# Optimization experiments

Hardware: AMD Instinct MI355X
Metric: run time of the kernel (lower is better)

The kernel has to match this reference:

```python
import jax, jax.numpy as jnp
import numpy as np

# dims: M=512 new tokens, N=2048 model dim, D=128 head dim, H=16 heads,
# L=4096 cache length, P=2048 cache write offset

def setup_inputs() -> dict:
    key = jax.random.key(0)
    k0, k1, k2, k3 = jax.random.split(key, 4)
    M, N, D, L = 512, 2048, 128, 4096
    X = jax.random.normal(k0, (M, N), jnp.float32)
    # scale weights ~1/sqrt(N) so projections have unit-ish scale
    W_qkv = jax.random.normal(k1, (N, 3 * N), jnp.float32) * (N ** -0.5)
    H = N // D
    cache_K = jax.random.normal(k2, (H, L, D), jnp.float32)
    # realistic cache state: keys stored in cache are RMS-normalized
    cache_K = cache_K * jax.lax.rsqrt(jnp.mean(cache_K * cache_K, axis=-1, keepdims=True))
    cache_V = jax.random.normal(k3, (H, L, D), jnp.float32)
    return {"X": X, "W_qkv": W_qkv, "cache_K": cache_K, "cache_V": cache_V, "P": 2048}


def reference(X, W_qkv, cache_K, cache_V, P):
    M = X.shape[0]
    H, L, D = cache_K.shape
    qkv = X @ W_qkv                              # [M, 3N]
    q, k, v = jnp.split(qkv, 3, axis=-1)         # each [M, N]
    q = q.reshape(M, H, D).transpose(1, 0, 2)    # [H, M, D]
    k = k.reshape(M, H, D).transpose(1, 0, 2)
    v = v.reshape(M, H, D).transpose(1, 0, 2)
    # RMS-style normalization (no learned gain, no eps in original)
    q = q * jax.lax.rsqrt(jnp.mean(q * q, axis=-1, keepdims=True))
    k = k * jax.lax.rsqrt(jnp.mean(k * k, axis=-1, keepdims=True))
    # scatter-update into KV cache at position P
    Kc = jax.lax.dynamic_update_slice(cache_K, k, (0, P, 0))  # [H, L, D]
    Vc = jax.lax.dynamic_update_slice(cache_V, v, (0, P, 0))
    # unmasked, unscaled attention over the full cache (faithful to original:
    # plain exp/sum, no max-subtraction, no 1/sqrt(D))
    scores = jnp.einsum('hmd,hld->hml', q, Kc)   # [H, M, L]
    w = jnp.exp(scores)
    w = w / jnp.sum(w, axis=-1, keepdims=True)
    out = jnp.einsum('hml,hld->hmd', w, Vc)      # [H, M, D]
    return out.transpose(1, 0, 2).reshape(M, H * D)
```

## Files before the change

### kernel.cpp

```cpp
#include <hip/hip_runtime.h>
#include <math.h>

typedef _Float16 half_t;
typedef _Float16 half8 __attribute__((ext_vector_type(8)));
typedef _Float16 half4_t __attribute__((ext_vector_type(4)));
typedef _Float16 half2_t __attribute__((ext_vector_type(2)));
typedef float floatx4 __attribute__((ext_vector_type(4)));

#define M_TOK 512
#define N_DIM 2048
#define D_HEAD 128
#define H_HEADS 16
#define L_CACHE 4096
#define THREE_N 6144
#define NCHUNK 16
#define LCHUNK 256

__global__ __launch_bounds__(256) void prep_kernel(const float* __restrict__ cK,
                                                   const float* __restrict__ cV,
                                                   const float* __restrict__ W,
                                                   const float* __restrict__ X,
                                                   half_t* __restrict__ K16,
                                                   half_t* __restrict__ V16T,
                                                   half_t* __restrict__ W16T,
                                                   half_t* __restrict__ X16) {
    __shared__ half_t tile[32 * 36];
    int b = blockIdx.x;
    int t = threadIdx.x;

    if (b < 8192) {
        size_t i = ((size_t)b * 256 + t) * 4;
        float4 v = *(const float4*)(cK + i);
        half4_t h = {(half_t)v.x, (half_t)v.y, (half_t)v.z, (half_t)v.w};
        *(half4_t*)(K16 + i) = h;
        return;
    }
    b -= 8192;
    if (b < 1024) {
        size_t i = ((size_t)b * 256 + t) * 4;
        float4 v = *(const float4*)(X + i);
        half4_t h = {(half_t)v.x, (half_t)v.y, (half_t)v.z, (half_t)v.w};
        *(half4_t*)(X16 + i) = h;
        return;
    }
    b -= 1024;
    if (b < 8192) {
        int h = b >> 9;
        int rem = b & 511;
        int lt = rem >> 2, dt = rem & 3;
        int l0 = lt * 32, d0 = dt * 32;
        {
            int li = t >> 3, c4 = (t & 7) * 4;
            float4 v = *(const float4*)(cV + ((size_t)h * L_CACHE + l0 + li) * D_HEAD + d0 + c4);
            tile[li * 36 + c4 + 0] = (half_t)v.x;
            tile[li * 36 + c4 + 1] = (half_t)v.y;
            tile[li * 36 + c4 + 2] = (half_t)v.z;
            tile[li * 36 + c4 + 3] = (half_t)v.w;
        }
        __syncthreads();
        {
            int di = t >> 3, lj = (t & 7) * 4;
            half4_t o = {tile[(lj + 0) * 36 + di], tile[(lj + 1) * 36 + di],
                         tile[(lj + 2) * 36 + di], tile[(lj + 3) * 36 + di]};
            *(half4_t*)(V16T + ((size_t)h * D_HEAD + d0 + di) * L_CACHE + l0 + lj) = o;
        }
        return;
    }
    b -= 8192;
    {
        int n0 = (b % 192) * 32, k0 = (b / 192) * 32;
        {
            int ki = t >> 3, n4 = (t & 7) * 4;
            float4 v = *(const float4*)(W + (size_t)(k0 + ki) * THREE_N + n0 + n4);
            tile[ki * 36 + n4 + 0] = (half_t)v.x;
            tile[ki * 36 + n4 + 1] = (half_t)v.y;
            tile[ki * 36 + n4 + 2] = (half_t)v.z;
            tile[ki * 36 + n4 + 3] = (half_t)v.w;
        }
        __syncthreads();
        {
            int ni = t >> 3, k4 = (t & 7) * 4;
            half4_t o = {tile[(k4 + 0) * 36 + ni], tile[(k4 + 1) * 36 + ni],
                         tile[(k4 + 2) * 36 + ni], tile[(k4 + 3) * 36 + ni]};
            *(half4_t*)(W16T + (size_t)(n0 + ni) * N_DIM + k0 + k4) = o;
        }
    }
}

__global__ __launch_bounds__(256) void gemm_fused_kernel(const half_t* __restrict__ X16,
                                                         const half_t* __restrict__ W16T,
                                                         const int* __restrict__ Pp,
                                                         half_t* __restrict__ Q16,
                                                         half_t* __restrict__ K16,
                                                         half_t* __restrict__ V16T) {
    __shared__ half_t As[64 * 72];
    __shared__ half_t Bs[128 * 72];
    __shared__ half_t Vt[128 * 72];
    __shared__ float ssbuf[4][32];
    const int t = threadIdx.x;
    const int wid = t >> 6, lane = t & 63;
    const int quad = lane >> 4, ln = lane & 15;
    const int bx = blockIdx.x, by = blockIdx.y;
    const int m0 = by * 64, n0 = bx * 128;
    const int wm = (wid >> 1) * 32, wn = (wid & 1) * 64;

    floatx4 acc[2][4] = {};

    const int ar = t >> 3, ag = (t & 7) * 8;
    const int br = t >> 3, bg = (t & 7) * 8;

    for (int k0 = 0; k0 < N_DIM; k0 += 64) {
        __syncthreads();
#pragma unroll
        for (int p = 0; p < 2; ++p) {
            int r = ar + p * 32;
            *(half8*)&As[r * 72 + ag] =
                *(const half8*)(X16 + (size_t)(m0 + r) * N_DIM + k0 + ag);
        }
#pragma unroll
        for (int p = 0; p < 4; ++p) {
            int r = br + p * 32;
            *(half8*)&Bs[r * 72 + bg] =
                *(const half8*)(W16T + (size_t)(n0 + r) * N_DIM + k0 + bg);
        }
        __syncthreads();
#pragma unroll
        for (int kt = 0; kt < 2; ++kt) {
            half8 a[2], b[4];
#pragma unroll
            for (int i = 0; i < 2; ++i)
                a[i] = *(half8*)&As[(wm + i * 16 + ln) * 72 + kt * 32 + quad * 8];
#pragma unroll
            for (int j = 0; j < 4; ++j)
                b[j] = *(half8*)&Bs[(wn + j * 16 + ln) * 72 + kt * 32 + quad * 8];
#pragma unroll
            for (int i = 0; i < 2; ++i)
#pragma unroll
                for (int j = 0; j < 4; ++j)
                    acc[i][j] = __builtin_amdgcn_mfma_f32_16x16x32_f16(a[i], b[j], acc[i][j], 0, 0, 0);
        }
    }

    const int seg = bx >> 4, h = bx & 15;
    const int P = *Pp;

    if (seg < 2) {
        float ss[2][4], scale[2][4];
#pragma unroll
        for (int i = 0; i < 2; ++i)
#pragma unroll
            for (int r = 0; r < 4; ++r) {
                float s = 0.f;
#pragma unroll
                for (int j = 0; j < 4; ++j) s += acc[i][j][r] * acc[i][j][r];
#pragma unroll
                for (int msk = 1; msk < 16; msk <<= 1) s += __shfl_xor(s, msk, 64);
                ss[i][r] = s;
            }
        if (ln == 0) {
#pragma unroll
            for (int i = 0; i < 2; ++i)
#pragma unroll
                for (int r = 0; r < 4; ++r)
                    ssbuf[wid][i * 16 + quad * 4 + r] = ss[i][r];
        }
        __syncthreads();
#pragma unroll
        for (int i = 0; i < 2; ++i)
#pragma unroll
            for (int r = 0; r < 4; ++r)
                scale[i][r] =
                    rsqrtf((ss[i][r] + ssbuf[wid ^ 1][i * 16 + quad * 4 + r]) * (1.0f / 128.0f));
#pragma unroll
        for (int i = 0; i < 2; ++i) {
            int mbase = m0 + wm + i * 16 + quad * 4;
#pragma unroll
            for (int j = 0; j < 4; ++j) {
                int col = wn + j * 16 + ln;
#pragma unroll
                for (int r = 0; r < 4; ++r) {
                    int m = mbase + r;
                    half_t val = (half_t)(acc[i][j][r] * scale[i][r]);
                    if (seg == 0)
                        Q16[((size_t)h * M_TOK + m) * D_HEAD + col] = val;
                    else
                        K16[((size_t)h * L_CACHE + P + m) * D_HEAD + col] = val;
                }
            }
        }
    } else {
#pragma unroll
        for (int i = 0; i < 2; ++i) {
            int mbase = wm + i * 16 + quad * 4;
#pragma unroll
            for (int j = 0; j < 4; ++j) {
                int d = wn + j * 16 + ln;
#pragma unroll
                for (int r = 0; r < 4; ++r)
                    Vt[d * 72 + mbase + r] = (half_t)acc[i][j][r];
            }
        }
        __syncthreads();
#pragma unroll
        for (int p = 0; p < 4; ++p) {
            int s = p * 256 + t;
            int d = s >> 3, sg = s & 7;
            *(half8*)(V16T + ((size_t)h * D_HEAD + d) * L_CACHE + P + m0 + sg * 8) =
                *(half8*)&Vt[d * 72 + sg * 8];
        }
    }
}

__global__ __launch_bounds__(256) void attn_partial_kernel(const half_t* __restrict__ Q16,
                                                           const half_t* __restrict__ K16,
                                                           const half_t* __restrict__ V16T,
                                                           half_t* __restrict__ Opart,
                                                           float* __restrict__ mstat,
                                                           float* __restrict__ lstat) {
    __shared__ half_t Ks[64 * 136];
    __shared__ half_t Vs[128 * 72];
    __shared__ half_t Ps[4 * 16 * 72];
    const int t = threadIdx.x, w = t >> 6, lane = t & 63;
    const int quad = lane >> 4, ln = lane & 15;
    const int h = blockIdx.y, c = blockIdx.z;
    const int mb = blockIdx.x * 128;
    const half_t* Qh = Q16 + (size_t)h * M_TOK * D_HEAD;
    const half_t* Kh = K16 + (size_t)h * L_CACHE * D_HEAD;
    const half_t* Vh = V16T + (size_t)h * D_HEAD * L_CACHE;

    half8 qf[2][4];
#pragma unroll
    for (int s = 0; s < 2; ++s) {
        int m0 = mb + s * 64 + w * 16;
#pragma unroll
        for (int dt = 0; dt < 4; ++dt)
            qf[s][dt] = *(const half8*)(Qh + (size_t)(m0 + ln) * D_HEAD + dt * 32 + quad * 8);
    }

    floatx4 oacc[2][8] = {};
    float mrow[2][4], lrow[2][4];
#pragma unroll
    for (int s = 0; s < 2; ++s)
#pragma unroll
        for (int r = 0; r < 4; ++r) { mrow[s][r] = -INFINITY; lrow[s][r] = 0.f; }

    half_t* Pw = Ps + w * (16 * 72);

    for (int l0 = c * LCHUNK; l0 < (c + 1) * LCHUNK; l0 += 64) {
        __syncthreads();
        {
            int lr = t >> 4, ch = t & 15;
#pragma unroll
            for (int p = 0; p < 4; ++p, lr += 16)
                *(half8*)&Ks[lr * 136 + ch * 8] =
                    *(const half8*)(Kh + (size_t)(l0 + lr) * D_HEAD + ch * 8);
        }
        {
            int dr = t >> 3, ch = t & 7;
#pragma unroll
            for (int p = 0; p < 4; ++p, dr += 32)
                *(half8*)&Vs[dr * 72 + ch * 8] =
                    *(const half8*)(Vh + (size_t)dr * L_CACHE + l0 + ch * 8);
        }
        __syncthreads();

#pragma unroll
        for (int s = 0; s < 2; ++s) {
            floatx4 sacc[4] = {};
#pragma unroll
            for (int nt = 0; nt < 4; ++nt)
#pragma unroll
                for (int dt = 0; dt < 4; ++dt) {
                    half8 b = *(half8*)&Ks[(nt * 16 + ln) * 136 + dt * 32 + quad * 8];
                    sacc[nt] = __builtin_amdgcn_mfma_f32_16x16x32_f16(qf[s][dt], b, sacc[nt], 0, 0, 0);
                }

            float alpha[4];
#pragma unroll
            for (int r = 0; r < 4; ++r) {
                float mx = fmaxf(fmaxf(sacc[0][r], sacc[1][r]), fmaxf(sacc[2][r], sacc[3][r]));
#pragma unroll
                for (int msk = 8; msk; msk >>= 1) mx = fmaxf(mx, __shfl_xor(mx, msk, 16));
                float mnew = fmaxf(mrow[s][r], mx);
                alpha[r] = __expf(mrow[s][r] - mnew);
                mrow[s][r] = mnew;
                float psum = 0.f;
#pragma unroll
                for (int nt = 0; nt < 4; ++nt) {
                    float p = __expf(sacc[nt][r] - mnew);
                    sacc[nt][r] = p;
                    psum += p;
                }
#pragma unroll
                for (int msk = 8; msk; msk >>= 1) psum += __shfl_xor(psum, msk, 16);
                lrow[s][r] = lrow[s][r] * alpha[r] + psum;
            }

#pragma unroll
            for (int nt = 0; nt < 4; ++nt)
#pragma unroll
                for (int r = 0; r < 4; ++r)
                    Pw[(quad * 4 + r) * 72 + nt * 16 + ln] = (half_t)sacc[nt][r];

#pragma unroll
            for (int nt8 = 0; nt8 < 8; ++nt8)
#pragma unroll
                for (int r = 0; r < 4; ++r)
                    oacc[s][nt8][r] *= alpha[r];

#pragma unroll
            for (int kt = 0; kt < 2; ++kt) {
                half8 a = *(half8*)&Pw[ln * 72 + kt * 32 + quad * 8];
#pragma unroll
                for (int nt8 = 0; nt8 < 8; ++nt8) {
                    half8 b = *(half8*)&Vs[(nt8 * 16 + ln) * 72 + kt * 32 + quad * 8];
                    oacc[s][nt8] = __builtin_amdgcn_mfma_f32_16x16x32_f16(a, b, oacc[s][nt8], 0, 0, 0);
                }
            }
        }
    }

    half_t* Oc = Opart + ((size_t)(c * H_HEADS + h) * M_TOK) * D_HEAD;
    float* ms = mstat + (size_t)(c * H_HEADS + h) * M_TOK;
    float* ls = lstat + (size_t)(c * H_HEADS + h) * M_TOK;
#pragma unroll
    for (int s = 0; s < 2; ++s) {
        int m0 = mb + s * 64 + w * 16;
#pragma unroll
        for (int nt8 = 0; nt8 < 8; ++nt8) {
            int col = nt8 * 16 + ln;
#pragma unroll
            for (int r = 0; r < 4; ++r)
                Oc[(size_t)(m0 + quad * 4 + r) * D_HEAD + col] = (half_t)oacc[s][nt8][r];
        }
        if (ln == 0) {
#pragma unroll
            for (int r = 0; r < 4; ++r) {
                ms[m0 + quad * 4 + r] = mrow[s][r];
                ls[m0 + quad * 4 + r] = lrow[s][r];
            }
        }
    }
}

__global__ __launch_bounds__(256) void combine_kernel(const half_t* __restrict__ Opart,
                                                      const float* __restrict__ mstat,
                                                      const float* __restrict__ lstat,
                                                      float* __restrict__ out) {
    int gw = blockIdx.x * 4 + (threadIdx.x >> 6);
    int lane = threadIdx.x & 63;
    int h = gw >> 9, m = gw & 511;
    int d = lane * 2;

    float ms[NCHUNK];
    float mg = -INFINITY;
#pragma unroll
    for (int c = 0; c < NCHUNK; ++c) {
        ms[c] = mstat[((c * H_HEADS + h) << 9) + m];
        mg = fmaxf(mg, ms[c]);
    }
    float denom = 0.f, o0 = 0.f, o1 = 0.f;
#pragma unroll
    for (int c = 0; c < NCHUNK; ++c) {
        float e = __expf(ms[c] - mg);
        denom += lstat[((c * H_HEADS + h) << 9) + m] * e;
        const half_t* Oc = Opart + (((size_t)(c * H_HEADS + h) << 9) + m) * D_HEAD + d;
        half2_t v = *(const half2_t*)Oc;
        o0 += (float)v.x * e;
        o1 += (float)v.y * e;
    }
    float inv = 1.0f / denom;
    float* op = out + (size_t)m * N_DIM + h * D_HEAD + d;
    op[0] = o0 * inv;
    op[1] = o1 * inv;
}

extern "C" void kernel_launch(void* const* d_in, const int* in_sizes, int n_in,
                              void* d_out, int out_size, void* d_ws, size_t ws_size,
                              hipStream_t stream) {
    const float* X = (const float*)d_in[0];
    const float* W = (const float*)d_in[1];
    const float* cK = (const float*)d_in[2];
    const float* cV = (const float*)d_in[3];
    const int* Pp = (const int*)d_in[4];
    float* out = (float*)d_out;

    char* ws = (char*)d_ws;
    half_t* Q16 = (half_t*)(ws + 0);
    half_t* K16 = (half_t*)(ws + 2097152);
    half_t* V16T = (half_t*)(ws + 18874368);
    half_t* X16 = (half_t*)(ws + 35651584);
    half_t* W16T = (half_t*)(ws + 37748736);
    half_t* Opart = (half_t*)(ws + 37748736);
    float* mstat = (float*)(ws + 71303168);
    float* lstat = (float*)(ws + 71827456);

    prep_kernel<<<29696, 256, 0, stream>>>(cK, cV, W, X, K16, V16T, W16T, X16);
    gemm_fused_kernel<<<dim3(48, 8), 256, 0, stream>>>(X16, W16T, Pp, Q16, K16, V16T);
    attn_partial_kernel<<<dim3(4, 16, NCHUNK), 256, 0, stream>>>(Q16, K16, V16T, Opart, mstat, lstat);
    combine_kernel<<<2048, 256, 0, stream>>>(Opart, mstat, lstat, out);
}
```

Before: 241.5 us.

## Restructure attention partial kernel: register prefetch, transposed QK, XCD-aware block mapping

Halves the number of split-L chunks (so each block handles 512 cache rows) and maps the flat block index so blocks sharing a head and chunk land on the same XCD, improving L2 reuse of K/V. K/V tiles are prefetched into registers while the current tile is computed. The QK MFMA is transposed so each lane owns one query row, which cuts the row max/sum shuffles to two steps, and the online-softmax rescale is skipped when the max does not grow. Risks include higher register pressure and fewer blocks for the combine step to merge against occupancy.

```diff
diff --git a/kernel.cpp b/kernel.cpp
--- a/kernel.cpp
+++ b/kernel.cpp
@@ -13,8 +13,8 @@
 #define H_HEADS 16
 #define L_CACHE 4096
 #define THREE_N 6144
-#define NCHUNK 16
-#define LCHUNK 256
+#define NCHUNK 8
+#define LCHUNK 512
 
 __global__ __launch_bounds__(256) void prep_kernel(const float* __restrict__ cK,
                                                    const float* __restrict__ cV,
@@ -219,11 +219,16 @@
                                                            float* __restrict__ lstat) {
     __shared__ half_t Ks[64 * 136];
     __shared__ half_t Vs[128 * 72];
-    __shared__ half_t Ps[4 * 16 * 72];
+    __shared__ half_t Ps[4 * 2 * 16 * 72];
     const int t = threadIdx.x, w = t >> 6, lane = t & 63;
     const int quad = lane >> 4, ln = lane & 15;
-    const int h = blockIdx.y, c = blockIdx.z;
-    const int mb = blockIdx.x * 128;
+
+    const int bid = blockIdx.x;
+    const int xcd = bid & 7, slot = bid >> 3;
+    const int pair = (xcd << 4) | (slot >> 2);
+    const int h = pair & 15, c = pair >> 4, mi = slot & 3;
+    const int mb = mi * 128;
+
     const half_t* Qh = Q16 + (size_t)h * M_TOK * D_HEAD;
     const half_t* Kh = K16 + (size_t)h * L_CACHE * D_HEAD;
     const half_t* Vh = V16T + (size_t)h * D_HEAD * L_CACHE;
@@ -231,91 +236,109 @@
     half8 qf[2][4];
 #pragma unroll
     for (int s = 0; s < 2; ++s) {
-        int m0 = mb + s * 64 + w * 16;
+        int m0 = mb + w * 32 + s * 16;
 #pragma unroll
         for (int dt = 0; dt < 4; ++dt)
             qf[s][dt] = *(const half8*)(Qh + (size_t)(m0 + ln) * D_HEAD + dt * 32 + quad * 8);
     }
 
     floatx4 oacc[2][8] = {};
-    float mrow[2][4], lrow[2][4];
-#pragma unroll
-    for (int s = 0; s < 2; ++s)
-#pragma unroll
-        for (int r = 0; r < 4; ++r) { mrow[s][r] = -INFINITY; lrow[s][r] = 0.f; }
-
-    half_t* Pw = Ps + w * (16 * 72);
-
-    for (int l0 = c * LCHUNK; l0 < (c + 1) * LCHUNK; l0 += 64) {
-        __syncthreads();
-        {
-            int lr = t >> 4, ch = t & 15;
-#pragma unroll
-            for (int p = 0; p < 4; ++p, lr += 16)
-                *(half8*)&Ks[lr * 136 + ch * 8] =
-                    *(const half8*)(Kh + (size_t)(l0 + lr) * D_HEAD + ch * 8);
-        }
-        {
-            int dr = t >> 3, ch = t & 7;
-#pragma unroll
-            for (int p = 0; p < 4; ++p, dr += 32)
-                *(half8*)&Vs[dr * 72 + ch * 8] =
-                    *(const half8*)(Vh + (size_t)dr * L_CACHE + l0 + ch * 8);
-        }
-        __syncthreads();
+    float mrow[2] = {-INFINITY, -INFINITY};
+    float lrow[2] = {0.f, 0.f};
+
+    half_t* Pw = Ps + w * (2 * 16 * 72);
+
+    const int l0base = c * LCHUNK;
+    const int kr = t >> 4, kc = (t & 15) * 8;
+    const int vr = t >> 3, vc = (t & 7) * 8;
+
+    half8 kreg[4], vreg[4];
+#pragma unroll
+    for (int p = 0; p < 4; ++p) {
+        kreg[p] = *(const half8*)(Kh + (size_t)(l0base + p * 16 + kr) * D_HEAD + kc);
+        vreg[p] = *(const half8*)(Vh + (size_t)(p * 32 + vr) * L_CACHE + l0base + vc);
+    }
+
+    for (int it = 0; it < LCHUNK / 64; ++it) {
+        __syncthreads();
+#pragma unroll
+        for (int p = 0; p < 4; ++p)
+            *(half8*)&Ks[(p * 16 + kr) * 136 + kc] = kreg[p];
+#pragma unroll
+        for (int p = 0; p < 4; ++p)
+            *(half8*)&Vs[(p * 32 + vr) * 72 + vc] = vreg[p];
+        if (it + 1 < LCHUNK / 64) {
+            int l1 = l0base + (it + 1) * 64;
+#pragma unroll
+            for (int p = 0; p < 4; ++p) {
+                kreg[p] = *(const half8*)(Kh + (size_t)(l1 + p * 16 + kr) * D_HEAD + kc);
+                vreg[p] = *(const half8*)(Vh + (size_t)(p * 32 + vr) * L_CACHE + l1 + vc);
+            }
+        }
+        __syncthreads();
+
+        floatx4 sacc[2][4] = {};
+#pragma unroll
+        for (int dt = 0; dt < 4; ++dt) {
+            half8 kf[4];
+#pragma unroll
+            for (int nt = 0; nt < 4; ++nt)
+                kf[nt] = *(half8*)&Ks[(nt * 16 + ln) * 136 + dt * 32 + quad * 8];
+#pragma unroll
+            for (int s = 0; s < 2; ++s)
+#pragma unroll
+                for (int nt = 0; nt < 4; ++nt)
+                    sacc[s][nt] = __builtin_amdgcn_mfma_f32_16x16x32_f16(kf[nt], qf[s][dt], sacc[s][nt], 0, 0, 0);
+        }
 
 #pragma unroll
         for (int s = 0; s < 2; ++s) {
-            floatx4 sacc[4] = {};
+            float mx = sacc[s][0][0];
 #pragma unroll
             for (int nt = 0; nt < 4; ++nt)
 #pragma unroll
-                for (int dt = 0; dt < 4; ++dt) {
-                    half8 b = *(half8*)&Ks[(nt * 16 + ln) * 136 + dt * 32 + quad * 8];
-                    sacc[nt] = __builtin_amdgcn_mfma_f32_16x16x32_f16(qf[s][dt], b, sacc[nt], 0, 0, 0);
+                for (int r = 0; r < 4; ++r) mx = fmaxf(mx, sacc[s][nt][r]);
+            mx = fmaxf(mx, __shfl_xor(mx, 16));
+            mx = fmaxf(mx, __shfl_xor(mx, 32));
+            if (__ballot(mx > mrow[s])) {
+                float mnew = fmaxf(mrow[s], mx);
+                float alpha = __expf(mrow[s] - mnew);
+                mrow[s] = mnew;
+                lrow[s] *= alpha;
+                float ar[4];
+#pragma unroll
+                for (int r = 0; r < 4; ++r) ar[r] = __shfl(alpha, quad * 4 + r, 16);
+#pragma unroll
+                for (int nt8 = 0; nt8 < 8; ++nt8)
+#pragma unroll
+                    for (int r = 0; r < 4; ++r) oacc[s][nt8][r] *= ar[r];
+            }
+            float psum = 0.f;
+#pragma unroll
+            for (int nt = 0; nt < 4; ++nt) {
+                half4_t h4;
+#pragma unroll
+                for (int r = 0; r < 4; ++r) {
+                    float p = __expf(sacc[s][nt][r] - mrow[s]);
+                    psum += p;
+                    h4[r] = (half_t)p;
                 }
-
-            float alpha[4];
-#pragma unroll
-            for (int r = 0; r < 4; ++r) {
-                float mx = fmaxf(fmaxf(sacc[0][r], sacc[1][r]), fmaxf(sacc[2][r], sacc[3][r]));
-#pragma unroll
-                for (int msk = 8; msk; msk >>= 1) mx = fmaxf(mx, __shfl_xor(mx, msk, 16));
-                float mnew = fmaxf(mrow[s][r], mx);
-                alpha[r] = __expf(mrow[s][r] - mnew);
-                mrow[s][r] = mnew;
-                float psum = 0.f;
-#pragma unroll
-                for (int nt = 0; nt < 4; ++nt) {
-                    float p = __expf(sacc[nt][r] - mnew);
-                    sacc[nt][r] = p;
-                    psum += p;
-                }
-#pragma unroll
-                for (int msk = 8; msk; msk >>= 1) psum += __shfl_xor(psum, msk, 16);
-                lrow[s][r] = lrow[s][r] * alpha[r] + psum;
-            }
-
-#pragma unroll
-            for (int nt = 0; nt < 4; ++nt)
-#pragma unroll
-                for (int r = 0; r < 4; ++r)
-                    Pw[(quad * 4 + r) * 72 + nt * 16 + ln] = (half_t)sacc[nt][r];
-
-#pragma unroll
-            for (int nt8 = 0; nt8 < 8; ++nt8)
-#pragma unroll
-                for (int r = 0; r < 4; ++r)
-                    oacc[s][nt8][r] *= alpha[r];
-
-#pragma unroll
-            for (int kt = 0; kt < 2; ++kt) {
-                half8 a = *(half8*)&Pw[ln * 72 + kt * 32 + quad * 8];
-#pragma unroll
-                for (int nt8 = 0; nt8 < 8; ++nt8) {
-                    half8 b = *(half8*)&Vs[(nt8 * 16 + ln) * 72 + kt * 32 + quad * 8];
-                    oacc[s][nt8] = __builtin_amdgcn_mfma_f32_16x16x32_f16(a, b, oacc[s][nt8], 0, 0, 0);
-                }
+                *(half4_t*)&Pw[s * 1152 + ln * 72 + nt * 16 + quad * 4] = h4;
+            }
+            psum += __shfl_xor(psum, 16);
+            psum += __shfl_xor(psum, 32);
+            lrow[s] += psum;
+        }
+
+#pragma unroll
+        for (int kt = 0; kt < 2; ++kt) {
+            half8 a0 = *(half8*)&Pw[ln * 72 + kt * 32 + quad * 8];
+            half8 a1 = *(half8*)&Pw[1152 + ln * 72 + kt * 32 + quad * 8];
+#pragma unroll
+            for (int nt8 = 0; nt8 < 8; ++nt8) {
+                half8 b = *(half8*)&Vs[(nt8 * 16 + ln) * 72 + kt * 32 + quad * 8];
+                oacc[0][nt8] = __builtin_amdgcn_mfma_f32_16x16x32_f16(a0, b, oacc[0][nt8], 0, 0, 0);
+                oacc[1][nt8] = __builtin_amdgcn_mfma_f32_16x16x32_f16(a1, b, oacc[1][nt8], 0, 0, 0);
             }
         }
     }
@@ -325,7 +348,7 @@
     float* ls = lstat + (size_t)(c * H_HEADS + h) * M_TOK;
 #pragma unroll
     for (int s = 0; s < 2; ++s) {
-        int m0 = mb + s * 64 + w * 16;
+        int m0 = mb + w * 32 + s * 16;
 #pragma unroll
         for (int nt8 = 0; nt8 < 8; ++nt8) {
             int col = nt8 * 16 + ln;
@@ -333,12 +356,9 @@
             for (int r = 0; r < 4; ++r)
                 Oc[(size_t)(m0 + quad * 4 + r) * D_HEAD + col] = (half_t)oacc[s][nt8][r];
         }
-        if (ln == 0) {
-#pragma unroll
-            for (int r = 0; r < 4; ++r) {
-                ms[m0 + quad * 4 + r] = mrow[s][r];
-                ls[m0 + quad * 4 + r] = lrow[s][r];
-            }
+        if (lane < 16) {
+            ms[m0 + lane] = mrow[s];
+            ls[m0 + lane] = lrow[s];
         }
     }
 }
@@ -397,6 +417,6 @@
 
     prep_kernel<<<29696, 256, 0, stream>>>(cK, cV, W, X, K16, V16T, W16T, X16);
     gemm_fused_kernel<<<dim3(48, 8), 256, 0, stream>>>(X16, W16T, Pp, Q16, K16, V16T);
-    attn_partial_kernel<<<dim3(4, 16, NCHUNK), 256, 0, stream>>>(Q16, K16, V16T, Opart, mstat, lstat);
+    attn_partial_kernel<<<512, 256, 0, stream>>>(Q16, K16, V16T, Opart, mstat, lstat);
     combine_kernel<<<2048, 256, 0, stream>>>(Opart, mstat, lstat, out);
 }
```

Measured after the change: 229.6 us. 4.9% less time.
